# Kernel tuning notes

Measured on AMD Instinct MI355X. Metric: run time of the kernel, lower is better.

Reference implementation:

```python
import jax, jax.numpy as jnp
import numpy as np

EPS = 1e-5
DN = ('NCHW', 'OIHW', 'NCHW')

def conv(x, w, b, stride, pad):
    y = jax.lax.conv_general_dilated(x, w, (stride, stride), [(pad, pad), (pad, pad)], dimension_numbers=DN)
    return y + b[None, :, None, None]

def instance_norm(x, gamma, beta):
    # normalize over spatial dims per (N, C)
    mu = jnp.mean(x, axis=(2, 3), keepdims=True)
    var = jnp.var(x, axis=(2, 3), keepdims=True)
    xh = (x - mu) * jax.lax.rsqrt(var + EPS)
    return xh * gamma[None, :, None, None] + beta[None, :, None, None]

def lrelu(x):
    return jnp.where(x >= 0, x, 0.2 * x)

def block(x, w, b, g, be, stride, pad):
    return lrelu(instance_norm(conv(x, w, b, stride, pad), g, be))

def setup_inputs() -> dict:
    key = jax.random.key(0)
    ks = jax.random.split(key, 16)
    dim = 64
    def rn(k, shape, s=0.05):
        return jax.random.normal(k, shape, dtype=jnp.float32) * s
    inp = {
        'x':   jax.random.normal(ks[0], (256, 3, 64, 64), dtype=jnp.float32),
        'w1': rn(ks[1], (dim, 3, 5, 5)),        'b1': jnp.zeros((dim,), jnp.float32),
        'g1': jnp.ones((dim,), jnp.float32),    'be1': jnp.zeros((dim,), jnp.float32),
        'w2': rn(ks[2], (dim*2, dim, 5, 5)),    'b2': jnp.zeros((dim*2,), jnp.float32),
        'g2': jnp.ones((dim*2,), jnp.float32),  'be2': jnp.zeros((dim*2,), jnp.float32),
        'w3': rn(ks[3], (dim*4, dim*2, 5, 5)),  'b3': jnp.zeros((dim*4,), jnp.float32),
        'g3': jnp.ones((dim*4,), jnp.float32),  'be3': jnp.zeros((dim*4,), jnp.float32),
        'w4': rn(ks[4], (dim*4, dim*4, 3, 3)),  'b4': jnp.zeros((dim*4,), jnp.float32),
        'g4': jnp.ones((dim*4,), jnp.float32),  'be4': jnp.zeros((dim*4,), jnp.float32),
        # MBD tensor T: (in_features=4096, out_features=64, kernel_dims=50), init N(0,1)
        'T':  jax.random.normal(ks[5], (4096, 64, 50), dtype=jnp.float32),
        'fc_w': rn(ks[6], (1000, 4096 + 64), s=0.02),
        'fc_b': jnp.zeros((1000,), jnp.float32),
    }
    return inp

def reference(x, w1, b1, g1, be1, w2, b2, g2, be2, w3, b3, g3, be3, w4, b4, g4, be4, T, fc_w, fc_b):
    bs = x.shape[0]
    f = block(x, w1, b1, g1, be1, 2, 2)   # (bs,64,32,32)
    f = block(f, w2, b2, g2, be2, 2, 2)   # (bs,128,16,16)
    f = block(f, w3, b3, g3, be3, 2, 2)   # (bs,256,8,8)
    f = block(f, w4, b4, g4, be4, 2, 1)   # (bs,256,4,4)
    feat = f.reshape(bs, -1)              # (bs,4096)
    # minibatch discrimination
    M = jnp.einsum('bi,iok->bok', feat, T)          # (bs,64,50)
    norm = jnp.sum(jnp.abs(M[None] - M[:, None]), axis=3)  # (bs,bs,64); [i,j]=|M_i-M_j|
    o_b = jnp.sum(jnp.exp(-norm), axis=0) - 1.0     # (bs,64)
    mb = jnp.concatenate([feat, o_b], axis=1)       # (bs,4160)
    y = mb @ fc_w.T + fc_b                          # (bs,1000)
    return feat, y
```

## Files before the change

### kernel.cpp

```cpp
#include <hip/hip_runtime.h>
#include <hip/hip_fp16.h>
#include <math.h>

#define EPSF 1e-5f

typedef __attribute__((ext_vector_type(4))) float  floatx4;
typedef __attribute__((ext_vector_type(4))) short  short4v;
typedef __attribute__((ext_vector_type(8))) short  short8v;

__device__ __forceinline__ unsigned short cvt_bf16(float f){
  unsigned u = __float_as_uint(f);
  unsigned r = (u + 0x7FFFu + ((u >> 16) & 1u)) >> 16;
  return (unsigned short)r;
}
__device__ __forceinline__ float bf2f(unsigned short h){
  return __uint_as_float(((unsigned)h) << 16);
}
__device__ __forceinline__ short8v ld_frag(const unsigned short* p){
  short4v lo = *(const short4v*)p;
  short4v hi = *(const short4v*)(p + 4);
  return __builtin_shufflevector(lo, hi, 0,1,2,3,4,5,6,7);
}
__device__ __forceinline__ float lrelu(float x){ return x >= 0.f ? x : 0.2f*x; }

__global__ __launch_bounds__(256) void prep_k(const float* __restrict__ w1, const float* __restrict__ w2,
                                              const float* __restrict__ w3, const float* __restrict__ w4,
                                              unsigned short* __restrict__ wb1, unsigned short* __restrict__ wb2,
                                              unsigned short* __restrict__ wb3, unsigned short* __restrict__ wb4,
                                              float* __restrict__ SQ){
  int b = blockIdx.x, t = threadIdx.x;
  if (b < 32){
    int idx = b*256 + t;
    int j = idx&7, lane = (idx>>3)&63, ks = (idx>>9)&3, grp = idx>>11;
    int co = grp*16 + (lane&15);
    int k = ks*32 + ((lane>>4)<<3) + j;
    int tap6 = k>>2, ci = k&3;
    int kh = tap6/6, kw = tap6 - kh*6;
    float v = 0.f;
    if (ci < 3 && kh < 5 && kw < 5) v = w1[(co*3 + ci)*25 + kh*5 + kw];
    wb1[idx] = cvt_bf16(v);
  } else if (b < 832){
    int idx = (b-32)*256 + t;
    int grp = idx/25600, rem = idx - grp*25600;
    int tap = rem/1024, rem2 = rem - tap*1024;
    int ccg = rem2>>9, lane = (rem2>>3)&63, j = rem2&7;
    int co = grp*16 + (lane&15);
    int ci = ccg*32 + ((lane>>4)<<3) + j;
    wb2[idx] = cvt_bf16(w2[(co*64 + ci)*25 + tap]);
  } else if (b < 4032){
    int idx = (b-832)*256 + t;
    int grp = idx/51200, rem = idx - grp*51200;
    int tap = rem/2048, rem2 = rem - tap*2048;
    int ccg = rem2>>9, lane = (rem2>>3)&63, j = rem2&7;
    int co = grp*16 + (lane&15);
    int ci = ccg*32 + ((lane>>4)<<3) + j;
    wb3[idx] = cvt_bf16(w3[(co*128 + ci)*25 + tap]);
  } else if (b < 6336){
    int idx = (b-4032)*256 + t;
    int grp = idx/36864, rem = idx - grp*36864;
    int tap = rem/4096, rem2 = rem - tap*4096;
    int ccg = rem2>>9, lane = (rem2>>3)&63, j = rem2&7;
    int co = grp*16 + (lane&15);
    int ci = ccg*32 + ((lane>>4)<<3) + j;
    wb4[idx] = cvt_bf16(w4[(co*256 + ci)*9 + tap]);
  } else {
    int idx = (b-6336)*256 + t;
    SQ[idx] = 0.f;
  }
}

__global__ __launch_bounds__(256) void packT_k(const float* __restrict__ T,
                                               unsigned short* __restrict__ Tp){
  const int b = blockIdx.x, t = threadIdx.x;
  __shared__ float tile[32][133];
  const int nb = b % 25, kt = b / 25;
  const int n0 = nb*128, k0 = kt*32;
  #pragma unroll
  for (int m=0;m<4;m++){
    int idx = m*256 + t;
    int row = idx>>5, c4 = (idx&31)<<2;
    const float4 v = *(const float4*)&T[(k0+row)*3200 + n0 + c4];
    tile[row][c4]   = v.x; tile[row][c4+1] = v.y;
    tile[row][c4+2] = v.z; tile[row][c4+3] = v.w;
  }
  __syncthreads();
  #pragma unroll
  for (int m=0;m<2;m++){
    int c = m*256 + t;
    int ngl = c>>6, lane = c&63, q = lane>>4, r = lane&15;
    unsigned short h[8];
    #pragma unroll
    for (int j=0;j<8;j++) h[j] = cvt_bf16(tile[q*8+j][ngl*16 + r]);
    *(uint4*)&Tp[(((nb*8 + ngl)*128 + kt)*64 + lane)*8] = *(const uint4*)h;
  }
}

__global__ __launch_bounds__(256) void packW_k(const float* __restrict__ W,
                                               unsigned short* __restrict__ Wp){
  int idx = blockIdx.x*256 + threadIdx.x;
  int lane = idx & 63, rem = idx >> 6;
  int kt = rem % 130, ng = rem / 130;
  int q = lane>>4, r = lane&15;
  int orow = ng*16 + r, k = kt*32 + (q<<3);
  unsigned short h[8] = {0,0,0,0,0,0,0,0};
  if (orow < 1000){
    float4 v0 = *(const float4*)&W[orow*4160 + k];
    float4 v1 = *(const float4*)&W[orow*4160 + k + 4];
    h[0]=cvt_bf16(v0.x); h[1]=cvt_bf16(v0.y); h[2]=cvt_bf16(v0.z); h[3]=cvt_bf16(v0.w);
    h[4]=cvt_bf16(v1.x); h[5]=cvt_bf16(v1.y); h[6]=cvt_bf16(v1.z); h[7]=cvt_bf16(v1.w);
  }
  *(uint4*)&Wp[idx*8] = *(const uint4*)h;
}

__global__ __launch_bounds__(256) void conv1_k(const float* __restrict__ x, const unsigned short* __restrict__ wb1P,
                                               float* __restrict__ S1, float* __restrict__ Q1,
                                               unsigned short* __restrict__ f1raw){
  const int t = threadIdx.x, n = blockIdx.x>>1, half = blockIdx.x&1;
  const int w = t>>6, lane = t&63, q = lane>>4, l16 = lane&15;
  __shared__ __align__(16) unsigned short img[36*68*4];
  short8v bf[4][4];
  #pragma unroll
  for (int nt=0;nt<4;nt++)
    #pragma unroll
    for (int ks=0;ks<4;ks++)
      bf[nt][ks] = *(const short8v*)&wb1P[((nt*4+ks)*64 + lane)*8];
  for (int i=t; i<4896; i+=256) ((unsigned*)img)[i] = 0u;
  __syncthreads();
  for (int idx=t; idx<1680; idx+=256){
    int ci = idx/560, rem = idx - ci*560;
    int tih = rem>>4, iw4 = (rem&15)<<2;
    int ih = half*32 - 2 + tih;
    if ((unsigned)ih < 64u){
      float4 v = *(const float4*)&x[((n*3+ci)<<12) + (ih<<6) + iw4];
      int base = (tih*68 + iw4 + 2)*4 + ci;
      img[base]    = cvt_bf16(v.x);
      img[base+4]  = cvt_bf16(v.y);
      img[base+8]  = cvt_bf16(v.z);
      img[base+12] = cvt_bf16(v.w);
    }
  }
  __syncthreads();
  floatx4 acc[8][4];
  #pragma unroll
  for (int mi=0;mi<8;mi++)
    #pragma unroll
    for (int nt=0;nt<4;nt++) acc[mi][nt] = (floatx4){0.f,0.f,0.f,0.f};
  #pragma unroll
  for (int mi=0; mi<8; mi++){
    int r = w*8 + mi;
    int ohl = r>>1, ow = ((r&1)<<4) + l16;
    #pragma unroll
    for (int ks=0; ks<4; ks++){
      int t0 = ks*8 + 2*q;
      int kh = t0/6, kw = t0 - kh*6;
      short8v a = ld_frag(&img[((ohl*2+kh)*68 + ow*2 + kw)*4]);
      #pragma unroll
      for (int nt=0; nt<4; nt++)
        acc[mi][nt] = __builtin_amdgcn_mfma_f32_16x16x32_bf16(a, bf[nt][ks], acc[mi][nt], 0,0,0);
    }
  }
  float sreg[4] = {0,0,0,0}, qreg[4] = {0,0,0,0};
  #pragma unroll
  for (int mi=0;mi<8;mi++){
    int r = w*8 + mi;
    #pragma unroll
    for (int nt=0;nt<4;nt++)
      #pragma unroll
      for (int e=0;e<4;e++){
        float v = acc[mi][nt][e];
        sreg[nt] += v; qreg[nt] += v*v;
        int px = half*512 + (r<<4) + (q<<2) + e;
        f1raw[(((n<<10)+px)<<6) + (nt<<4) + l16] = cvt_bf16(v);
      }
  }
  #pragma unroll
  for (int nt=0;nt<4;nt++){
    float s = sreg[nt], qq = qreg[nt];
    s  += __shfl_xor(s,16,64);  s  += __shfl_xor(s,32,64);
    qq += __shfl_xor(qq,16,64); qq += __shfl_xor(qq,32,64);
    if (q==0){
      atomicAdd(&S1[(n<<6) + (nt<<4) + l16], s);
      atomicAdd(&Q1[(n<<6) + (nt<<4) + l16], qq);
    }
  }
}

__global__ __launch_bounds__(512) void conv2_k(const unsigned short* __restrict__ fin,
                                               const unsigned short* __restrict__ wbP,
                                               const float* __restrict__ S1, const float* __restrict__ Q1,
                                               const float* __restrict__ g1, const float* __restrict__ be1,
                                               float* __restrict__ S2, float* __restrict__ Q2,
                                               unsigned short* __restrict__ fout){
  const int t = threadIdx.x;
  const int n = blockIdx.x >> 1, half = blockIdx.x & 1;
  const int w = t>>6, lane = t&63, q = lane>>4, l16 = lane&15;
  const int rw = w&1, cw = w>>1;
  __shared__ __align__(16) unsigned short tile[684*40];
  __shared__ float gmA[64], btA[64];
  if (t < 64){
    float S = S1[(n<<6)+t], Q = Q1[(n<<6)+t];
    float mu = S*(1.f/1024.f), var = fmaxf(Q*(1.f/1024.f) - mu*mu, 0.f);
    float r = rsqrtf(var+EPSF)*g1[t];
    gmA[t] = r; btA[t] = be1[t] - mu*r;
  }
  __syncthreads();
  floatx4 acc[4][2];
  #pragma unroll
  for (int mt=0;mt<4;mt++)
    #pragma unroll
    for (int nt=0;nt<2;nt++) acc[mt][nt] = (floatx4){0.f,0.f,0.f,0.f};
  int cellb[4];
  #pragma unroll
  for (int mt=0;mt<4;mt++){
    int r = rw*64 + mt*16 + l16;
    int ohl = r>>4, ow = r&15;
    cellb[mt] = (2*ohl)*36 + 2*ow;
  }
  for (int ccg = 0; ccg < 2; ccg++){
    const int cc = ccg<<5;
    if (ccg) __syncthreads();
    #pragma unroll
    for (int it=0; it<6; it++){
      int idx = it*512 + t;
      if (idx < 2736){
        int cell = idx>>2, s = idx&3;
        int s2 = s ^ ((cell>>3)&1);
        int ci0 = s<<3;
        int tih = cell/36, tiw = cell - tih*36;
        int ih = half*16 + tih - 2, iw = tiw - 2;
        uint4 v = {0u,0u,0u,0u};
        if ((unsigned)ih < 32u && (unsigned)iw < 32u){
          v = *(const uint4*)&fin[(((n*32+ih)*32 + iw)<<6) + cc + ci0];
          unsigned short* hp = (unsigned short*)&v;
          #pragma unroll
          for (int jj=0;jj<8;jj++){
            int c = cc + ci0 + jj;
            hp[jj] = cvt_bf16(lrelu(bf2f(hp[jj])*gmA[c]+btA[c]));
          }
        }
        *(uint4*)&tile[cell*40 + (s2<<3)] = v;
      }
    }
    __syncthreads();
    const unsigned short* bp[2];
    #pragma unroll
    for (int nt=0;nt<2;nt++)
      bp[nt] = wbP + ((((cw*2+nt)*25)*2 + ccg)<<9) + lane*8;
    short8v bq[2][4];
    #pragma unroll
    for (int p=0;p<4;p++)
      #pragma unroll
      for (int nt=0;nt<2;nt++) bq[nt][p] = *(const short8v*)(bp[nt] + (p<<10));
    #pragma unroll
    for (int tap=0; tap<25; tap++){
      const int kh = tap/5, kw = tap - kh*5;
      const int aoff = kh*36 + kw;
      short8v a[4];
      #pragma unroll
      for (int mt=0;mt<4;mt++){
        int cell = cellb[mt] + aoff;
        int q2 = q ^ ((cell>>3)&1);
        a[mt] = *(const short8v*)&tile[cell*40 + q2*8];
      }
      #pragma unroll
      for (int mt=0;mt<4;mt++)
        #pragma unroll
        for (int nt=0;nt<2;nt++)
          acc[mt][nt] = __builtin_amdgcn_mfma_f32_16x16x32_bf16(a[mt], bq[nt][tap&3], acc[mt][nt], 0,0,0);
      if (tap+4 < 25){
        #pragma unroll
        for (int nt=0;nt<2;nt++) bq[nt][tap&3] = *(const short8v*)(bp[nt] + ((tap+4)<<10));
      }
    }
  }
  #pragma unroll
  for (int nt=0;nt<2;nt++){
    int co = cw*32 + nt*16 + l16;
    float s=0.f, qq=0.f;
    #pragma unroll
    for (int mt=0;mt<4;mt++)
      #pragma unroll
      for (int e=0;e<4;e++){ float xv = acc[mt][nt][e]; s += xv; qq += xv*xv; }
    s  += __shfl_xor(s,16,64);  s  += __shfl_xor(s,32,64);
    qq += __shfl_xor(qq,16,64); qq += __shfl_xor(qq,32,64);
    if (q == 0){
      atomicAdd(&S2[n*128 + co], s);
      atomicAdd(&Q2[n*128 + co], qq);
    }
    #pragma unroll
    for (int mt=0;mt<4;mt++)
      #pragma unroll
      for (int e=0;e<4;e++){
        int px = half*128 + rw*64 + mt*16 + q*4 + e;
        fout[((n<<8) + px)*128 + co] = cvt_bf16(acc[mt][nt][e]);
      }
  }
}

__global__ __launch_bounds__(512) void conv3_k(const unsigned short* __restrict__ fin,
                                               const unsigned short* __restrict__ wbP,
                                               const float* __restrict__ S2, const float* __restrict__ Q2,
                                               const float* __restrict__ g2, const float* __restrict__ be2,
                                               const float* __restrict__ g, const float* __restrict__ be,
                                               unsigned short* __restrict__ fout){
  const int t = threadIdx.x, n = blockIdx.x, co0 = blockIdx.y<<7;
  const int w = t>>6, lane = t&63, q = lane>>4, l16 = lane&15;
  const int rw = w&1, cw = w>>1;
  __shared__ __align__(16) unsigned short tile[361*40];
  __shared__ float gmA[128], btA[128];
  __shared__ float SQs[2][128], SQq[2][128];
  if (t < 128){
    float S = S2[n*128+t], Q = Q2[n*128+t];
    float mu = S*(1.f/256.f), var = fmaxf(Q*(1.f/256.f) - mu*mu, 0.f);
    float r = rsqrtf(var+EPSF)*g2[t];
    gmA[t] = r; btA[t] = be2[t] - mu*r;
  }
  __syncthreads();
  floatx4 acc[2][2];
  #pragma unroll
  for (int mt=0;mt<2;mt++)
    #pragma unroll
    for (int nt=0;nt<2;nt++) acc[mt][nt] = (floatx4){0.f,0.f,0.f,0.f};
  int cellb[2];
  #pragma unroll
  for (int mt=0;mt<2;mt++){
    int r = rw*32 + mt*16 + l16;
    int oh = r>>3, ow = r&7;
    cellb[mt] = (2*oh)*19 + 2*ow;
  }
  for (int ccg = 0; ccg < 4; ccg++){
    const int cc = ccg<<5;
    if (ccg) __syncthreads();
    #pragma unroll
    for (int it=0; it<3; it++){
      int idx = it*512 + t;
      if (idx < 1444){
        int cell = idx>>2, s = idx&3;
        int s2 = s ^ ((cell>>3)&1);
        int ci0 = s<<3;
        int tih = cell/19, tiw = cell - tih*19;
        int ih = tih - 2, iw = tiw - 2;
        uint4 v = {0u,0u,0u,0u};
        if ((unsigned)ih < 16u && (unsigned)iw < 16u){
          v = *(const uint4*)&fin[(((n*16+ih)*16 + iw)<<7) + cc + ci0];
          unsigned short* hp = (unsigned short*)&v;
          #pragma unroll
          for (int jj=0;jj<8;jj++){
            int c = cc + ci0 + jj;
            hp[jj] = cvt_bf16(lrelu(bf2f(hp[jj])*gmA[c]+btA[c]));
          }
        }
        *(uint4*)&tile[cell*40 + (s2<<3)] = v;
      }
    }
    __syncthreads();
    const unsigned short* bp[2];
    #pragma unroll
    for (int nt=0;nt<2;nt++)
      bp[nt] = wbP + (((((co0>>4)+cw*2+nt)*25)*4 + ccg)<<9) + lane*8;
    short8v bq[2][4];
    #pragma unroll
    for (int p=0;p<4;p++)
      #pragma unroll
      for (int nt=0;nt<2;nt++) bq[nt][p] = *(const short8v*)(bp[nt] + (p<<11));
    #pragma unroll
    for (int tap=0; tap<25; tap++){
      const int kh = tap/5, kw = tap - kh*5;
      const int aoff = kh*19 + kw;
      short8v a[2];
      #pragma unroll
      for (int mt=0;mt<2;mt++){
        int cell = cellb[mt] + aoff;
        int q2 = q ^ ((cell>>3)&1);
        a[mt] = *(const short8v*)&tile[cell*40 + q2*8];
      }
      #pragma unroll
      for (int mt=0;mt<2;mt++)
        #pragma unroll
        for (int nt=0;nt<2;nt++)
          acc[mt][nt] = __builtin_amdgcn_mfma_f32_16x16x32_bf16(a[mt], bq[nt][tap&3], acc[mt][nt], 0,0,0);
      if (tap+4 < 25){
        #pragma unroll
        for (int nt=0;nt<2;nt++) bq[nt][tap&3] = *(const short8v*)(bp[nt] + ((tap+4)<<11));
      }
    }
  }
  #pragma unroll
  for (int nt=0;nt<2;nt++){
    int lcol = cw*32 + nt*16 + l16;
    float s=0.f, qq=0.f;
    #pragma unroll
    for (int mt=0;mt<2;mt++)
      #pragma unroll
      for (int e=0;e<4;e++){ float xv = acc[mt][nt][e]; s += xv; qq += xv*xv; }
    s  += __shfl_xor(s,16,64);  s  += __shfl_xor(s,32,64);
    qq += __shfl_xor(qq,16,64); qq += __shfl_xor(qq,32,64);
    if (q == 0){ SQs[rw][lcol] = s; SQq[rw][lcol] = qq; }
  }
  __syncthreads();
  #pragma unroll
  for (int nt=0;nt<2;nt++){
    int lcol = cw*32 + nt*16 + l16, co = co0 + lcol;
    float S = SQs[0][lcol] + SQs[1][lcol];
    float Q = SQq[0][lcol] + SQq[1][lcol];
    float mu = S*(1.f/64.f), var = fmaxf(Q*(1.f/64.f) - mu*mu, 0.f);
    float gmv = rsqrtf(var+EPSF)*g[co];
    float btv = be[co] - mu*gmv;
    #pragma unroll
    for (int mt=0;mt<2;mt++)
      #pragma unroll
      for (int e=0;e<4;e++){
        int row = rw*32 + mt*16 + q*4 + e;
        fout[((n<<6) + row)*256 + co] = cvt_bf16(lrelu(acc[mt][nt][e]*gmv+btv));
      }
  }
}

__global__ __launch_bounds__(256) void conv4_k(const unsigned short* __restrict__ fin,
                                               const unsigned short* __restrict__ wbP,
                                               const float* __restrict__ g, const float* __restrict__ be,
                                               float* __restrict__ feat, unsigned short* __restrict__ featb){
  const int t = threadIdx.x;
  const int n0 = blockIdx.x << 1, co0 = blockIdx.y << 6;
  const int w = t>>6, lane = t&63, q = lane>>4, l16 = lane&15;
  const int rw = w&1, cw = w>>1;
  __shared__ __align__(16) unsigned short tile[2*81*40];
  floatx4 acc[2];
  acc[0] = (floatx4){0.f,0.f,0.f,0.f};
  acc[1] = (floatx4){0.f,0.f,0.f,0.f};
  const int oh = l16>>2, ow = l16&3;
  const int cellb = (2*oh)*9 + 2*ow;
  for (int ccg = 0; ccg < 8; ccg++){
    const int cc = ccg<<5;
    if (ccg) __syncthreads();
    #pragma unroll
    for (int it=0; it<3; it++){
      int idx = it*256 + t;
      if (idx < 648){
        int img = idx >= 324 ? 1 : 0;
        int rem = idx - img*324;
        int cell = rem>>2, s = rem&3;
        int fc = img*81 + cell;
        int s2 = s ^ ((fc>>3)&1);
        int ci0 = s<<3;
        int tih = cell/9, tiw = cell - tih*9;
        int ih = tih - 1, iw = tiw - 1;
        uint4 v = {0u,0u,0u,0u};
        if ((unsigned)ih < 8u && (unsigned)iw < 8u)
          v = *(const uint4*)&fin[((((n0+img)*8+ih)*8 + iw)<<8) + cc + ci0];
        *(uint4*)&tile[fc*40 + (s2<<3)] = v;
      }
    }
    __syncthreads();
    const unsigned short* bp[2];
    #pragma unroll
    for (int nt=0;nt<2;nt++)
      bp[nt] = wbP + (((((co0>>4)+cw*2+nt)*9)*8 + ccg)<<9) + lane*8;
    short8v bq[2][4];
    #pragma unroll
    for (int p=0;p<4;p++)
      #pragma unroll
      for (int nt=0;nt<2;nt++) bq[nt][p] = *(const short8v*)(bp[nt] + (p<<12));
    #pragma unroll
    for (int tap=0; tap<9; tap++){
      const int kh = tap/3, kw = tap - kh*3;
      int fc = rw*81 + cellb + kh*9 + kw;
      int q2 = q ^ ((fc>>3)&1);
      short8v a = *(const short8v*)&tile[fc*40 + q2*8];
      #pragma unroll
      for (int nt=0;nt<2;nt++)
        acc[nt] = __builtin_amdgcn_mfma_f32_16x16x32_bf16(a, bq[nt][tap&3], acc[nt], 0,0,0);
      if (tap+4 < 9){
        #pragma unroll
        for (int nt=0;nt<2;nt++) bq[nt][tap&3] = *(const short8v*)(bp[nt] + ((tap+4)<<12));
      }
    }
  }
  const int nn = n0 + rw;
  #pragma unroll
  for (int nt=0;nt<2;nt++){
    int co = co0 + cw*32 + nt*16 + l16;
    float s=0.f, qq=0.f;
    #pragma unroll
    for (int e=0;e<4;e++){ float xv = acc[nt][e]; s += xv; qq += xv*xv; }
    s  += __shfl_xor(s,16,64);  s  += __shfl_xor(s,32,64);
    qq += __shfl_xor(qq,16,64); qq += __shfl_xor(qq,32,64);
    float mu = s*(1.f/16.f), var = fmaxf(qq*(1.f/16.f) - mu*mu, 0.f);
    float gmv = rsqrtf(var+EPSF)*g[co];
    float btv = be[co] - mu*gmv;
    #pragma unroll
    for (int e=0;e<4;e++){
      int px = q*4 + e;
      float vv = lrelu(acc[nt][e]*gmv+btv);
      feat [(nn<<12) + (co<<4) + px] = vv;
      featb[(nn<<12) + (co<<4) + px] = cvt_bf16(vv);
    }
  }
}

__global__ __launch_bounds__(256) void gemmM_k(const unsigned short* __restrict__ A,
                                               const unsigned short* __restrict__ Tp,
                                               float* __restrict__ Cp){
  const int t = threadIdx.x;
  const int n0 = blockIdx.x<<7, b0 = blockIdx.y<<7, k0 = blockIdx.z<<9;
  const int w = t>>6, lane = t&63, q = lane>>4, l16 = lane&15;
  const int rw = w&1, cw = w>>1;
  floatx4 acc[4][4];
  #pragma unroll
  for (int mt=0;mt<4;mt++)
    #pragma unroll
    for (int nt=0;nt<4;nt++) acc[mt][nt] = (floatx4){0.f,0.f,0.f,0.f};
  const unsigned short* Ab[4];
  const unsigned short* Bb[4];
  #pragma unroll
  for (int mt=0;mt<4;mt++)
    Ab[mt] = A + (b0 + (rw<<6) + (mt<<4) + l16)*4096 + k0 + (q<<3);
  #pragma unroll
  for (int nt=0;nt<4;nt++)
    Bb[nt] = Tp + ((((n0>>4) + (cw<<2) + nt)*128 + (k0>>5))*64 + lane)*8;
  #pragma unroll 4
  for (int kt=0; kt<16; kt++){
    short8v af[4], bfr[4];
    #pragma unroll
    for (int mt=0;mt<4;mt++) af[mt] = *(const short8v*)(Ab[mt] + kt*32);
    #pragma unroll
    for (int nt=0;nt<4;nt++) bfr[nt] = *(const short8v*)(Bb[nt] + kt*512);
    #pragma unroll
    for (int mt=0;mt<4;mt++)
      #pragma unroll
      for (int nt=0;nt<4;nt++)
        acc[mt][nt] = __builtin_amdgcn_mfma_f32_16x16x32_bf16(af[mt], bfr[nt], acc[mt][nt], 0,0,0);
  }
  float* C = Cp + blockIdx.z * 819200;
  #pragma unroll
  for (int mt=0;mt<4;mt++)
    #pragma unroll
    for (int nt=0;nt<4;nt++)
      #pragma unroll
      for (int e=0;e<4;e++){
        int row = b0 + (rw<<6) + (mt<<4) + (q<<2) + e;
        int col = n0 + (cw<<6) + (nt<<4) + l16;
        C[row*3200 + col] = acc[mt][nt][e];
      }
}

__global__ __launch_bounds__(256) void reduceM_k(const float* __restrict__ Cp, __half* __restrict__ Mh){
  int idx = blockIdx.x*256 + threadIdx.x;
  if (idx >= 917504) return;
  int i = idx / 3584, r = idx - i*3584;
  int o = r / 56, k = r - o*56;
  float v = 0.f;
  if (k < 50){
    int src = i*3200 + o*50 + k;
    #pragma unroll
    for (int s = 0; s < 8; s++) v += Cp[s*819200 + src];
  }
  Mh[idx] = __float2half(v);
}

__global__ __launch_bounds__(256) void pair_k(const __half* __restrict__ Mh,
                                              float* __restrict__ ob, unsigned short* __restrict__ obb){
  const int j = blockIdx.x, t = threadIdx.x;
  __shared__ __align__(16) __half2 Mj[1792];
  __shared__ float red[256];
  for (int k=t; k<448; k+=256) ((uint4*)Mj)[k] = ((const uint4*)&Mh[j*3584])[k];
  __syncthreads();
  const int o = t & 63, ss = t >> 6;
  const uint4* mjp4 = (const uint4*)&Mj[o*28];
  float sum = 0.f;
  for (int i = ss<<6; i < (ss<<6)+64; i++){
    const uint4* mip4 = (const uint4*)&Mh[i*3584 + o*56];
    __half2 acch = __float2half2_rn(0.f);
    #pragma unroll
    for (int u=0;u<7;u++){
      uint4 av = mip4[u], bv = mjp4[u];
      const __half2* ah = (const __half2*)&av;
      const __half2* bh = (const __half2*)&bv;
      #pragma unroll
      for (int e=0;e<4;e++)
        acch = __hadd2(acch, __habs2(__hsub2(ah[e], bh[e])));
    }
    float dsum = __low2float(acch) + __high2float(acch);
    sum += __expf(-dsum);
  }
  red[(o<<2)+ss] = sum;
  __syncthreads();
  if (t < 64){
    float v = red[t<<2] + red[(t<<2)+1] + red[(t<<2)+2] + red[(t<<2)+3] - 1.0f;
    ob[(j<<6)+t] = v;
    obb[(j<<6)+t] = cvt_bf16(v);
  }
}

__global__ __launch_bounds__(256) void gemmFC_k(const unsigned short* __restrict__ featb,
                                                const unsigned short* __restrict__ obb,
                                                const unsigned short* __restrict__ Wp,
                                                float* __restrict__ Cp){
  const int t = threadIdx.x;
  const int o0 = blockIdx.x<<7, b0 = blockIdx.y<<7, kz = blockIdx.z;
  const int w = t>>6, lane = t&63, q = lane>>4, l16 = lane&15;
  const int rw = w&1, cw = w>>1;
  floatx4 acc[4][4];
  #pragma unroll
  for (int mt=0;mt<4;mt++)
    #pragma unroll
    for (int nt=0;nt<4;nt++) acc[mt][nt] = (floatx4){0.f,0.f,0.f,0.f};
  int rowb[4];
  #pragma unroll
  for (int mt=0;mt<4;mt++) rowb[mt] = b0 + (rw<<6) + (mt<<4) + l16;
  const unsigned short* Bb[4];
  #pragma unroll
  for (int nt=0;nt<4;nt++)
    Bb[nt] = Wp + ((((o0>>4) + (cw<<2) + nt)*130 + kz*10)*64 + lane)*8;
  #pragma unroll 2
  for (int kt=0; kt<10; kt++){
    int k = kz*320 + kt*32 + (q<<3);
    short8v af[4], bfr[4];
    #pragma unroll
    for (int mt=0;mt<4;mt++)
      af[mt] = (k < 4096) ? *(const short8v*)&featb[rowb[mt]*4096 + k]
                          : *(const short8v*)&obb[rowb[mt]*64 + (k-4096)];
    #pragma unroll
    for (int nt=0;nt<4;nt++) bfr[nt] = *(const short8v*)(Bb[nt] + kt*512);
    #pragma unroll
    for (int mt=0;mt<4;mt++)
      #pragma unroll
      for (int nt=0;nt<4;nt++)
        acc[mt][nt] = __builtin_amdgcn_mfma_f32_16x16x32_bf16(af[mt], bfr[nt], acc[mt][nt], 0,0,0);
  }
  float* C = Cp + blockIdx.z * 256000;
  #pragma unroll
  for (int mt=0;mt<4;mt++)
    #pragma unroll
    for (int nt=0;nt<4;nt++)
      #pragma unroll
      for (int e=0;e<4;e++){
        int row = b0 + (rw<<6) + (mt<<4) + (q<<2) + e;
        int col = o0 + (cw<<6) + (nt<<4) + l16;
        if (col < 1000) C[row*1000 + col] = acc[mt][nt][e];
      }
}

__global__ __launch_bounds__(256) void reduceY_k(const float* __restrict__ Cp, const float* __restrict__ bias,
                                                 float* __restrict__ y){
  int idx = blockIdx.x * 256 + threadIdx.x;
  if (idx >= 256000) return;
  int o = idx % 1000;
  float r = bias[o];
  #pragma unroll
  for (int s = 0; s < 13; s++) r += Cp[s*256000 + idx];
  y[idx] = r;
}

extern "C" void kernel_launch(void* const* d_in, const int* in_sizes, int n_in,
                              void* d_out, int out_size, void* d_ws, size_t ws_size,
                              hipStream_t stream){
  const float* x   = (const float*)d_in[0];
  const float* w1  = (const float*)d_in[1];
  const float* g1  = (const float*)d_in[3];
  const float* be1 = (const float*)d_in[4];
  const float* w2  = (const float*)d_in[5];
  const float* g2  = (const float*)d_in[7];
  const float* be2 = (const float*)d_in[8];
  const float* w3  = (const float*)d_in[9];
  const float* g3  = (const float*)d_in[11];
  const float* be3 = (const float*)d_in[12];
  const float* w4  = (const float*)d_in[13];
  const float* g4  = (const float*)d_in[15];
  const float* be4 = (const float*)d_in[16];
  const float* T   = (const float*)d_in[17];
  const float* fcw = (const float*)d_in[18];
  const float* fcb = (const float*)d_in[19];
  float* out = (float*)d_out;
  float* ws  = (float*)d_ws;

  unsigned short* f1raw = (unsigned short*)ws;
  unsigned short* Tp    = (unsigned short*)ws;
  unsigned short* f2    = (unsigned short*)(ws + 8388608);
  unsigned short* f3    = (unsigned short*)(ws + 12582912);
  unsigned short* featb = (unsigned short*)(ws + 14680064);
  unsigned short* wb1   = (unsigned short*)(ws + 15204352);
  unsigned short* wb2   = (unsigned short*)(ws + 15208448);
  unsigned short* wb3   = (unsigned short*)(ws + 15310848);
  unsigned short* wb4   = (unsigned short*)(ws + 15720448);
  float* S1    = ws + 16015360;
  float* Q1    = ws + 16031744;
  float* S2    = ws + 16048128;
  float* Q2    = ws + 16080896;
  float* Mp    = ws + 16113664;
  unsigned short* Wp  = (unsigned short*)(ws + 16113664);
  __half* Mh   = (__half*)(ws + 22667264);
  float* obuf  = ws + 23126016;
  unsigned short* obb = (unsigned short*)(ws + 23142400);
  float* yp    = ws + 23150592;
  float* feat  = out;
  float* y     = out + 1048576;

  prep_k<<<dim3(6720), 256, 0, stream>>>(w1, w2, w3, w4, wb1, wb2, wb3, wb4, S1);

  conv1_k<<<dim3(512),     256, 0, stream>>>(x, wb1, S1, Q1, f1raw);
  conv2_k<<<dim3(512),     512, 0, stream>>>(f1raw, wb2, S1, Q1, g1, be1, S2, Q2, f2);
  packT_k<<<dim3(3200),    256, 0, stream>>>(T, Tp);
  conv3_k<<<dim3(256, 2),  512, 0, stream>>>(f2, wb3, S2, Q2, g2, be2, g3, be3, f3);
  conv4_k<<<dim3(128, 4),  256, 0, stream>>>(f3, wb4, g4, be4, feat, featb);

  gemmM_k  <<<dim3(25, 2, 8),  256, 0, stream>>>(featb, Tp, Mp);
  reduceM_k<<<dim3(3584),      256, 0, stream>>>(Mp, Mh);
  packW_k  <<<dim3(2080),      256, 0, stream>>>(fcw, Wp);
  pair_k   <<<dim3(256),       256, 0, stream>>>(Mh, obuf, obb);
  gemmFC_k <<<dim3(8, 2, 13),  256, 0, stream>>>(featb, obb, Wp, yp);
  reduceY_k<<<dim3(1000),      256, 0, stream>>>(yp, fcb, y);
}
```

Measured before the change: 394.2 us.

## Split pairwise MBD kernel over i-chunks with register prefetch and separate reduction

The pairwise L1/exp kernel now uses a 2D grid (64 j-groups × 8 i-chunks) instead of 256 blocks. Each thread holds its M_j row in registers rather than shared memory and prefetches the next M_i row into registers. The half2 accumulation is split into four independent chains to shorten the dependency path. Partial sums go to a new workspace buffer that a small finalize kernel reduces and converts to bf16. This adds a kernel launch, extra global traffic and higher register pressure in exchange for more parallelism and latency hiding.

```diff
diff --git a/kernel.cpp b/kernel.cpp
--- a/kernel.cpp
+++ b/kernel.cpp
@@ -558,38 +558,52 @@
   Mh[idx] = __float2half(v);
 }
 
-__global__ __launch_bounds__(256) void pair_k(const __half* __restrict__ Mh,
-                                              float* __restrict__ ob, unsigned short* __restrict__ obb){
-  const int j = blockIdx.x, t = threadIdx.x;
-  __shared__ __align__(16) __half2 Mj[1792];
-  __shared__ float red[256];
-  for (int k=t; k<448; k+=256) ((uint4*)Mj)[k] = ((const uint4*)&Mh[j*3584])[k];
-  __syncthreads();
-  const int o = t & 63, ss = t >> 6;
-  const uint4* mjp4 = (const uint4*)&Mj[o*28];
+__global__ __launch_bounds__(256) void pairv2_k(const __half* __restrict__ Mh,
+                                                float* __restrict__ obp){
+  const int t = threadIdx.x, jb = blockIdx.x, ib = blockIdx.y;
+  const int o = t & 63, jj = t >> 6;
+  const int j = jb*4 + jj;
+  const uint4* M4 = (const uint4*)Mh;
+  uint4 mj[7];
+  #pragma unroll
+  for (int u=0;u<7;u++) mj[u] = M4[j*448 + o*7 + u];
+  const int i0 = ib*32;
+  uint4 cur[7], nxt[7];
+  #pragma unroll
+  for (int u=0;u<7;u++) cur[u] = M4[i0*448 + o*7 + u];
   float sum = 0.f;
-  for (int i = ss<<6; i < (ss<<6)+64; i++){
-    const uint4* mip4 = (const uint4*)&Mh[i*3584 + o*56];
-    __half2 acch = __float2half2_rn(0.f);
+  for (int ii=0; ii<32; ii++){
+    if (ii < 31){
+      #pragma unroll
+      for (int u=0;u<7;u++) nxt[u] = M4[(i0+ii+1)*448 + o*7 + u];
+    }
+    __half2 a0 = __float2half2_rn(0.f), a1 = a0, a2 = a0, a3 = a0;
     #pragma unroll
     for (int u=0;u<7;u++){
-      uint4 av = mip4[u], bv = mjp4[u];
-      const __half2* ah = (const __half2*)&av;
-      const __half2* bh = (const __half2*)&bv;
-      #pragma unroll
-      for (int e=0;e<4;e++)
-        acch = __hadd2(acch, __habs2(__hsub2(ah[e], bh[e])));
-    }
-    float dsum = __low2float(acch) + __high2float(acch);
+      const __half2* ah = (const __half2*)&cur[u];
+      const __half2* bh = (const __half2*)&mj[u];
+      a0 = __hadd2(a0, __habs2(__hsub2(ah[0], bh[0])));
+      a1 = __hadd2(a1, __habs2(__hsub2(ah[1], bh[1])));
+      a2 = __hadd2(a2, __habs2(__hsub2(ah[2], bh[2])));
+      a3 = __hadd2(a3, __habs2(__hsub2(ah[3], bh[3])));
+    }
+    __half2 s01 = __hadd2(a0, a1), s23 = __hadd2(a2, a3);
+    __half2 s = __hadd2(s01, s23);
+    float dsum = __low2float(s) + __high2float(s);
     sum += __expf(-dsum);
-  }
-  red[(o<<2)+ss] = sum;
-  __syncthreads();
-  if (t < 64){
-    float v = red[t<<2] + red[(t<<2)+1] + red[(t<<2)+2] + red[(t<<2)+3] - 1.0f;
-    ob[(j<<6)+t] = v;
-    obb[(j<<6)+t] = cvt_bf16(v);
-  }
+    #pragma unroll
+    for (int u=0;u<7;u++) cur[u] = nxt[u];
+  }
+  obp[ib*16384 + jb*256 + t] = sum;
+}
+
+__global__ __launch_bounds__(256) void finalizeOB_k(const float* __restrict__ obp,
+                                                    unsigned short* __restrict__ obb){
+  int idx = blockIdx.x*256 + threadIdx.x;
+  float v = -1.0f;
+  #pragma unroll
+  for (int s=0;s<8;s++) v += obp[s*16384 + idx];
+  obb[idx] = cvt_bf16(v);
 }
 
 __global__ __launch_bounds__(256) void gemmFC_k(const unsigned short* __restrict__ featb,
@@ -690,9 +704,9 @@
   float* Mp    = ws + 16113664;
   unsigned short* Wp  = (unsigned short*)(ws + 16113664);
   __half* Mh   = (__half*)(ws + 22667264);
-  float* obuf  = ws + 23126016;
   unsigned short* obb = (unsigned short*)(ws + 23142400);
   float* yp    = ws + 23150592;
+  float* obp   = ws + 26478592;
   float* feat  = out;
   float* y     = out + 1048576;
 
@@ -707,7 +721,8 @@
   gemmM_k  <<<dim3(25, 2, 8),  256, 0, stream>>>(featb, Tp, Mp);
   reduceM_k<<<dim3(3584),      256, 0, stream>>>(Mp, Mh);
   packW_k  <<<dim3(2080),      256, 0, stream>>>(fcw, Wp);
-  pair_k   <<<dim3(256),       256, 0, stream>>>(Mh, obuf, obb);
+  pairv2_k <<<dim3(64, 8),     256, 0, stream>>>(Mh, obp);
+  finalizeOB_k<<<dim3(64),     256, 0, stream>>>(obp, obb);
   gemmFC_k <<<dim3(8, 2, 13),  256, 0, stream>>>(featb, obb, Wp, yp);
   reduceY_k<<<dim3(1000),      256, 0, stream>>>(yp, fcb, y);
 }
```

New measurement: 354.2 us. 1.11x faster.
